# Performance work log

Measured on AMD Instinct MI355X. Metric: run time of the kernel, lower is better.

The kernel has to match this reference:

```python
import jax, jax.numpy as jnp
import numpy as np

# ActivationWithGain: activation scaled so a standard-normal input keeps unit variance.
_s = np.random.default_rng(0).standard_normal(1 << 20).astype(np.float32)
GAIN = float(1.0 / (_s / (1.0 + np.exp(-_s))).std())  # SiLU gain ~ 1.787
INV_SQRT2 = np.float32(1.0 / np.sqrt(2.0))


def _act(x):
    return jax.nn.silu(x) * jnp.float32(GAIN)


def setup_inputs() -> dict:
    key = jax.random.key(0)
    ks = jax.random.split(key, 9)
    n_up, n_dn, n_nuc, dim, edim = 512, 512, 256, 256, 32
    n_el = n_up + n_dn
    n_edges = n_el * n_nuc  # dense electron-nucleus bipartite graph
    return {
        "elec_emb": jax.random.normal(ks[0], (n_el, dim), jnp.float32),
        "up_inp": jax.random.normal(ks[1], (n_nuc, dim), jnp.float32),
        "down_inp": jax.random.normal(ks[2], (n_nuc, dim), jnp.float32),
        "edge_emb": jax.random.normal(ks[3], (n_edges, edim), jnp.float32),
        "contr": jax.random.uniform(ks[4], (n_edges,), jnp.float32),
        "norm": jax.random.uniform(ks[5], (n_el,), jnp.float32),
        "W_out": jax.random.normal(ks[6], (dim, dim), jnp.float32) / np.float32(np.sqrt(dim)),
        "b_out": jnp.zeros((dim,), jnp.float32),
        "W_edge": jax.random.normal(ks[7], (edim, dim), jnp.float32) / np.float32(np.sqrt(edim)),
        "W_out2": jax.random.normal(ks[8], (dim, dim), jnp.float32) / np.float32(np.sqrt(dim)),
        "b_out2": jnp.zeros((dim,), jnp.float32),
        "scale1": jnp.ones((), jnp.float32),  # FixedScalingFactor (frozen after init)
        "scale2": jnp.ones((), jnp.float32),
        "n_up": n_up,
        "n_down": n_dn,
        "n_nuclei": n_nuc,
    }


def reference(elec_emb, up_inp, down_inp, edge_emb, contr, norm,
              W_out, b_out, W_edge, W_out2, b_out2, scale1, scale2,
              n_up, n_down, n_nuclei):
    n_el = n_up + n_down
    # adj_idx for a single graph: dense bipartite edges, sorted by electron index
    e_n_i = jnp.repeat(jnp.arange(n_el), n_nuclei)   # [E] electron index per edge
    e_n_k = jnp.tile(jnp.arange(n_nuclei), n_el)     # [E] nucleus index per edge

    out_emb = elec_emb @ W_out + b_out               # Dense(out_dim)

    mask = jnp.arange(n_el) < n_up                   # spin_mask: True for spin-up electrons
    e_n_mask = mask[e_n_i]
    # gather nuclear embeddings per edge, selecting up/down table by electron spin
    inp = jnp.where(e_n_mask[:, None], up_inp[e_n_k], down_inp[e_n_k])  # [E, D]

    weights = edge_emb @ W_edge                      # Dense_no_bias(out_dim), [E, D]
    # FixedScalingFactor: contr only weights the init-time variance estimate;
    # at runtime the op is x * scale1.
    to_elec = inp * weights * scale1                 # [E, D]

    agg = jax.ops.segment_sum(to_elec, e_n_i, num_segments=n_el,
                              indices_are_sorted=True)  # [n_el, D]
    out_emb = (out_emb + agg * norm[:, None]) * scale2
    out_emb = _act(out_emb)
    out_emb = _act(out_emb @ W_out2 + b_out2)
    # residual: shapes match, so rescaled sum
    return (elec_emb + out_emb) * INV_SQRT2
```

## Files before the change

### kernel.cpp

```cpp
#include <hip/hip_runtime.h>
#include <hip/hip_bf16.h>

#define N_EL   1024
#define N_UP   512
#define NNUC   256
#define DIM    256
#define EDIM   32
#define KTOT   8192
#define NKP    8

#define GAIN_F      1.7872135f
#define INV_SQRT2_F 0.7071067811865476f

typedef __attribute__((ext_vector_type(8))) short bf16x8;
typedef __attribute__((ext_vector_type(4))) short bf16x4;
typedef __attribute__((ext_vector_type(4))) float f32x4;

__device__ __forceinline__ short f2bf(float x) {
    union { __hip_bfloat16 h; short s; } u;
    u.h = __float2bfloat16(x);
    return u.s;
}

__global__ __launch_bounds__(256) void prep_kernel(
    const float* __restrict__ up, const float* __restrict__ dn,
    const float* __restrict__ wedge,
    const float* __restrict__ w1, const float* __restrict__ w2,
    const float* __restrict__ elec,
    short* __restrict__ w1f, short* __restrict__ w2f,
    short* __restrict__ elecb, short* __restrict__ Tf)
{
    const int idx = (blockIdx.x << 8) + threadIdx.x;

    if (idx < 65536) {
        {
            const int b  = idx & 7;
            const int l  = (idx >> 3) & 63;
            const int q  = (idx >> 9) & 7;
            const int nt = idx >> 12;
            const int j  = (q << 5) + ((l >> 4) << 3) + b;
            const int d  = (nt << 4) + (l & 15);
            w1f[idx] = f2bf(w1[j * DIM + d]);
            w2f[idx] = f2bf(w2[j * DIM + d]);
        }
        {
            const f32x4 v = *(const f32x4*)(elec + (idx << 2));
            bf16x4 o;
            o[0] = f2bf(v[0]); o[1] = f2bf(v[1]);
            o[2] = f2bf(v[2]); o[3] = f2bf(v[3]);
            *(bf16x4*)(elecb + (idx << 2)) = o;
        }
    }

    {
        const int s   = idx >> 18;
        const int rem = idx & 262143;
        const int kt  = rem >> 10;
        const int dt  = (rem >> 6) & 15;
        const int l   = rem & 63;
        const int d   = (dt << 4) + (l & 15);
        const int jb  = (l >> 4) << 3;
        const float* __restrict__ inp = s ? dn : up;
        const float iv = inp[kt * DIM + d];
        const float* __restrict__ wcol = wedge + d;
        bf16x8 o;
        #pragma unroll
        for (int b = 0; b < 8; ++b)
            o[b] = f2bf(iv * wcol[(jb + b) * DIM]);
        *(bf16x8*)(Tf + ((size_t)s << 21) + ((size_t)rem << 3)) = o;
    }
}

__global__ __launch_bounds__(512) void edge_gemm(
    const float* __restrict__ eemb,
    const short* __restrict__ Tf,
    float* __restrict__ P)
{
    __shared__ short A_lds[2][4096];

    const int tid  = threadIdx.x;
    const int w    = tid >> 6;
    const int lane = tid & 63;
    const int g    = lane >> 4;
    const int c    = lane & 15;
    const int kp   = blockIdx.x & 7;
    const int rt   = blockIdx.x >> 3;
    const int rb   = rt << 5;
    const int kb   = kp << 10;

    const short* __restrict__ Tb = Tf + ((rb < N_UP) ? 0 : (1 << 21));

    const int f  = w;
    const int r_ = f >> 2;
    const int q_ = f & 3;
    const float* __restrict__ Asrc = eemb
        + (size_t)(rb + (r_ << 4) + c) * KTOT
        + kb + (q_ << 5) + (g << 3);

    f32x4 s_lo, s_hi;
    bf16x8 bA[8], bB[8];

    auto STAGE_LOAD = [&](int sub) {
        const float* p = Asrc + (sub << 7);
        s_lo = *(const f32x4*)p;
        s_hi = *(const f32x4*)(p + 4);
    };
    auto STAGE_WRITE = [&](int buf) {
        union { bf16x8 v; short s[8]; } o;
        o.s[0] = f2bf(s_lo[0]); o.s[1] = f2bf(s_lo[1]);
        o.s[2] = f2bf(s_lo[2]); o.s[3] = f2bf(s_lo[3]);
        o.s[4] = f2bf(s_hi[0]); o.s[5] = f2bf(s_hi[1]);
        o.s[6] = f2bf(s_hi[2]); o.s[7] = f2bf(s_hi[3]);
        *(bf16x8*)(&A_lds[buf][(f << 9) + (lane << 3)]) = o.v;
    };
    auto LOADB = [&](int sub, bf16x8 (&bd)[8]) {
        #pragma unroll
        for (int t = 0; t < 2; ++t) {
            const int ct = (w << 1) + t;
            #pragma unroll
            for (int q = 0; q < 4; ++q) {
                const int ktg = (kp << 5) + (sub << 2) + q;
                bd[(t << 2) + q] = *(const bf16x8*)(
                    Tb + (((((ktg << 4) + ct) << 6) + lane) << 3));
            }
        }
    };

    f32x4 acc[2][2] = {{{0.f,0.f,0.f,0.f},{0.f,0.f,0.f,0.f}},
                       {{0.f,0.f,0.f,0.f},{0.f,0.f,0.f,0.f}}};

    auto COMPUTE = [&](int buf, bf16x8 (&bc)[8]) {
        bf16x8 a[2][4];
        #pragma unroll
        for (int rr = 0; rr < 2; ++rr)
            #pragma unroll
            for (int q = 0; q < 4; ++q)
                a[rr][q] = *(const bf16x8*)(
                    &A_lds[buf][((((rr << 2) + q)) << 9) + (lane << 3)]);
        #pragma unroll
        for (int q = 0; q < 4; ++q) {
            acc[0][0] = __builtin_amdgcn_mfma_f32_16x16x32_bf16(a[0][q], bc[q],     acc[0][0], 0, 0, 0);
            acc[0][1] = __builtin_amdgcn_mfma_f32_16x16x32_bf16(a[0][q], bc[4 + q], acc[0][1], 0, 0, 0);
            acc[1][0] = __builtin_amdgcn_mfma_f32_16x16x32_bf16(a[1][q], bc[q],     acc[1][0], 0, 0, 0);
            acc[1][1] = __builtin_amdgcn_mfma_f32_16x16x32_bf16(a[1][q], bc[4 + q], acc[1][1], 0, 0, 0);
        }
    };

    STAGE_LOAD(0);
    LOADB(0, bA);
    STAGE_WRITE(0);
    __syncthreads();

    #pragma unroll
    for (int sub = 0; sub < 8; ++sub) {
        if ((sub & 1) == 0) {
            if (sub < 7) { STAGE_LOAD(sub + 1); LOADB(sub + 1, bB); }
            COMPUTE(0, bA);
        } else {
            if (sub < 7) { STAGE_LOAD(sub + 1); LOADB(sub + 1, bA); }
            COMPUTE(1, bB);
        }
        if (sub < 7) STAGE_WRITE((sub & 1) ^ 1);
        __syncthreads();
    }

    float* __restrict__ Pp = P + ((size_t)kp << 18);
    #pragma unroll
    for (int rr = 0; rr < 2; ++rr)
        #pragma unroll
        for (int t = 0; t < 2; ++t) {
            const int ct = (w << 1) + t;
            #pragma unroll
            for (int j = 0; j < 4; ++j) {
                const int row = rb + (rr << 4) + (g << 2) + j;
                Pp[(row << 8) + (ct << 4) + c] = acc[rr][t][j];
            }
        }
}

__global__ __launch_bounds__(256) void reduce_kernel(
    const float* __restrict__ P,
    const float* __restrict__ s1p,
    float* __restrict__ agg)
{
    const int idx = (blockIdx.x << 8) + threadIdx.x;
    const float s1 = *s1p;
    f32x4 s = {0.f, 0.f, 0.f, 0.f};
    #pragma unroll
    for (int kp = 0; kp < NKP; ++kp) {
        const f32x4 v = *(const f32x4*)(P + ((size_t)kp << 18) + (idx << 2));
        s[0] += v[0]; s[1] += v[1]; s[2] += v[2]; s[3] += v[3];
    }
    s[0] *= s1; s[1] *= s1; s[2] *= s1; s[3] *= s1;
    *(f32x4*)(agg + (idx << 2)) = s;
}

__global__ __launch_bounds__(512) void out_kernel(
    const short* __restrict__ elecb,
    const short* __restrict__ w1f, const short* __restrict__ w2f,
    const float* __restrict__ elec, const float* __restrict__ agg,
    const float* __restrict__ norm,
    const float* __restrict__ b1, const float* __restrict__ b2,
    const float* __restrict__ s2p,
    float* __restrict__ outp)
{
    __shared__ short h_s[16][264];

    const int tid  = threadIdx.x;
    const int w    = tid >> 6;
    const int lane = tid & 63;
    const int g    = lane >> 4;
    const int c    = lane & 15;
    const int mt   = blockIdx.x >> 2;
    const int qd   = blockIdx.x & 3;
    const int mb   = mt << 4;

    const short* abase = elecb + ((mb + c) << 8) + (g << 3);
    bf16x8 a[8];
    #pragma unroll
    for (int q = 0; q < 8; ++q) a[q] = *(const bf16x8*)(abase + (q << 5));

    const float s2 = *s2p;

    #pragma unroll
    for (int t = 0; t < 2; ++t) {
        const int ct = (w << 1) + t;
        const short* bb = w1f + (ct << 12) + (lane << 3);
        bf16x8 b[8];
        #pragma unroll
        for (int q = 0; q < 8; ++q) b[q] = *(const bf16x8*)(bb + (q << 9));
        f32x4 acc = {0.f, 0.f, 0.f, 0.f};
        #pragma unroll
        for (int q = 0; q < 8; ++q)
            acc = __builtin_amdgcn_mfma_f32_16x16x32_bf16(a[q], b[q], acc, 0, 0, 0);

        const int n  = (ct << 4) + c;
        const float bv = b1[n];
        #pragma unroll
        for (int r = 0; r < 4; ++r) {
            const int mr = (g << 2) + r;
            const int m  = mb + mr;
            const float y = (acc[r] + bv + agg[(m << 8) + n] * norm[m]) * s2;
            const float sig = 1.f / (1.f + __expf(-y));
            h_s[mr][n] = f2bf(GAIN_F * y * sig);
        }
    }
    __syncthreads();

    if (w < 4) {
        bf16x8 a2[8];
        #pragma unroll
        for (int q = 0; q < 8; ++q)
            a2[q] = *(const bf16x8*)(&h_s[c][(q << 5) + (g << 3)]);

        const int ct = (qd << 2) + w;
        const short* bb = w2f + (ct << 12) + (lane << 3);
        bf16x8 b[8];
        #pragma unroll
        for (int q = 0; q < 8; ++q) b[q] = *(const bf16x8*)(bb + (q << 9));
        f32x4 acc = {0.f, 0.f, 0.f, 0.f};
        #pragma unroll
        for (int q = 0; q < 8; ++q)
            acc = __builtin_amdgcn_mfma_f32_16x16x32_bf16(a2[q], b[q], acc, 0, 0, 0);

        const int n  = (ct << 4) + c;
        const float bv = b2[n];
        #pragma unroll
        for (int r = 0; r < 4; ++r) {
            const int m = mb + (g << 2) + r;
            const float z = acc[r] + bv;
            const float sig = 1.f / (1.f + __expf(-z));
            const float o = GAIN_F * z * sig;
            outp[(m << 8) + n] = (elec[(m << 8) + n] + o) * INV_SQRT2_F;
        }
    }
}

extern "C" void kernel_launch(void* const* d_in, const int* in_sizes, int n_in,
                              void* d_out, int out_size, void* d_ws, size_t ws_size,
                              hipStream_t stream)
{
    const float* elec  = (const float*)d_in[0];
    const float* up    = (const float*)d_in[1];
    const float* dn    = (const float*)d_in[2];
    const float* eemb  = (const float*)d_in[3];
    const float* norm  = (const float*)d_in[5];
    const float* W1    = (const float*)d_in[6];
    const float* b1    = (const float*)d_in[7];
    const float* Wedge = (const float*)d_in[8];
    const float* W2    = (const float*)d_in[9];
    const float* b2    = (const float*)d_in[10];
    const float* s1    = (const float*)d_in[11];
    const float* s2    = (const float*)d_in[12];

    short* sbase = (short*)d_ws;
    short* w1f   = sbase;
    short* w2f   = sbase + 65536;
    short* elecb = sbase + 131072;
    short* Tf    = sbase + 393216;
    float* P     = (float*)(sbase + 393216 + 4194304);
    float* agg   = P + (size_t)NKP * 262144;

    prep_kernel  <<<2048, 256, 0, stream>>>(up, dn, Wedge, W1, W2, elec,
                                            w1f, w2f, elecb, Tf);
    edge_gemm    <<<256, 512, 0, stream>>>(eemb, Tf, P);
    reduce_kernel<<<256, 256, 0, stream>>>(P, s1, agg);
    out_kernel   <<<256, 512, 0, stream>>>(elecb, w1f, w2f, elec, agg, norm,
                                           b1, b2, s2, (float*)d_out);
}
```

Before: 30.99 us.

## Pre-convert edge embeddings to MFMA-tiled bf16 in prep, drop LDS staging

The fp32 edge_emb matrix is now converted once in the prep kernel into a bf16 layout already tiled for MFMA fragments. The edge GEMM then loads A fragments straight from global memory into registers with double buffering, which removes the LDS staging buffer and the per-step __syncthreads. The cost is an extra full pass over the 32 MB fp32 input to write a 16 MB bf16 copy, plus twice as many prep blocks. Since the GEMM reads A only once per block anyway, the extra traffic may outweigh the sync savings.

```diff
diff --git a/kernel.cpp b/kernel.cpp
--- a/kernel.cpp
+++ b/kernel.cpp
@@ -26,9 +26,10 @@
     const float* __restrict__ up, const float* __restrict__ dn,
     const float* __restrict__ wedge,
     const float* __restrict__ w1, const float* __restrict__ w2,
-    const float* __restrict__ elec,
+    const float* __restrict__ elec, const float* __restrict__ eemb,
     short* __restrict__ w1f, short* __restrict__ w2f,
-    short* __restrict__ elecb, short* __restrict__ Tf)
+    short* __restrict__ elecb, short* __restrict__ Tf,
+    short* __restrict__ eembb)
 {
     const int idx = (blockIdx.x << 8) + threadIdx.x;
 
@@ -52,7 +53,7 @@
         }
     }
 
-    {
+    if (idx < 524288) {
         const int s   = idx >> 18;
         const int rem = idx & 262143;
         const int kt  = rem >> 10;
@@ -69,15 +70,30 @@
             o[b] = f2bf(iv * wcol[(jb + b) * DIM]);
         *(bf16x8*)(Tf + ((size_t)s << 21) + ((size_t)rem << 3)) = o;
     }
+
+    {
+        const int mt16 = idx >> 14;
+        const int kt   = (idx >> 6) & 255;
+        const int l    = idx & 63;
+        const int row  = (mt16 << 4) + (l & 15);
+        const int kk   = (kt << 5) + ((l >> 4) << 3);
+        const float* src = eemb + (size_t)row * KTOT + kk;
+        const f32x4 lo = *(const f32x4*)src;
+        const f32x4 hi = *(const f32x4*)(src + 4);
+        bf16x8 o;
+        o[0] = f2bf(lo[0]); o[1] = f2bf(lo[1]);
+        o[2] = f2bf(lo[2]); o[3] = f2bf(lo[3]);
+        o[4] = f2bf(hi[0]); o[5] = f2bf(hi[1]);
+        o[6] = f2bf(hi[2]); o[7] = f2bf(hi[3]);
+        *(bf16x8*)(eembb + ((size_t)idx << 3)) = o;
+    }
 }
 
 __global__ __launch_bounds__(512) void edge_gemm(
-    const float* __restrict__ eemb,
+    const short* __restrict__ eembb,
     const short* __restrict__ Tf,
     float* __restrict__ P)
 {
-    __shared__ short A_lds[2][4096];
-
     const int tid  = threadIdx.x;
     const int w    = tid >> 6;
     const int lane = tid & 63;
@@ -86,32 +102,20 @@
     const int kp   = blockIdx.x & 7;
     const int rt   = blockIdx.x >> 3;
     const int rb   = rt << 5;
-    const int kb   = kp << 10;
 
     const short* __restrict__ Tb = Tf + ((rb < N_UP) ? 0 : (1 << 21));
 
-    const int f  = w;
-    const int r_ = f >> 2;
-    const int q_ = f & 3;
-    const float* __restrict__ Asrc = eemb
-        + (size_t)(rb + (r_ << 4) + c) * KTOT
-        + kb + (q_ << 5) + (g << 3);
-
-    f32x4 s_lo, s_hi;
-    bf16x8 bA[8], bB[8];
-
-    auto STAGE_LOAD = [&](int sub) {
-        const float* p = Asrc + (sub << 7);
-        s_lo = *(const f32x4*)p;
-        s_hi = *(const f32x4*)(p + 4);
-    };
-    auto STAGE_WRITE = [&](int buf) {
-        union { bf16x8 v; short s[8]; } o;
-        o.s[0] = f2bf(s_lo[0]); o.s[1] = f2bf(s_lo[1]);
-        o.s[2] = f2bf(s_lo[2]); o.s[3] = f2bf(s_lo[3]);
-        o.s[4] = f2bf(s_hi[0]); o.s[5] = f2bf(s_hi[1]);
-        o.s[6] = f2bf(s_hi[2]); o.s[7] = f2bf(s_hi[3]);
-        *(bf16x8*)(&A_lds[buf][(f << 9) + (lane << 3)]) = o.v;
+    auto LOADA = [&](int sub, bf16x8 (&ad)[2][4]) {
+        #pragma unroll
+        for (int rr = 0; rr < 2; ++rr) {
+            const int mt16 = (rt << 1) + rr;
+            #pragma unroll
+            for (int q = 0; q < 4; ++q) {
+                const int kt = (kp << 5) + (sub << 2) + q;
+                ad[rr][q] = *(const bf16x8*)(
+                    eembb + ((size_t)(((mt16 << 8) + kt) << 6) + lane) * 8);
+            }
+        }
     };
     auto LOADB = [&](int sub, bf16x8 (&bd)[8]) {
         #pragma unroll
@@ -129,14 +133,7 @@
     f32x4 acc[2][2] = {{{0.f,0.f,0.f,0.f},{0.f,0.f,0.f,0.f}},
                        {{0.f,0.f,0.f,0.f},{0.f,0.f,0.f,0.f}}};
 
-    auto COMPUTE = [&](int buf, bf16x8 (&bc)[8]) {
-        bf16x8 a[2][4];
-        #pragma unroll
-        for (int rr = 0; rr < 2; ++rr)
-            #pragma unroll
-            for (int q = 0; q < 4; ++q)
-                a[rr][q] = *(const bf16x8*)(
-                    &A_lds[buf][((((rr << 2) + q)) << 9) + (lane << 3)]);
+    auto COMPUTE = [&](bf16x8 (&a)[2][4], bf16x8 (&bc)[8]) {
         #pragma unroll
         for (int q = 0; q < 4; ++q) {
             acc[0][0] = __builtin_amdgcn_mfma_f32_16x16x32_bf16(a[0][q], bc[q],     acc[0][0], 0, 0, 0);
@@ -146,22 +143,20 @@
         }
     };
 
-    STAGE_LOAD(0);
+    bf16x8 aA[2][4], aB[2][4], bA[8], bB[8];
+
+    LOADA(0, aA);
     LOADB(0, bA);
-    STAGE_WRITE(0);
-    __syncthreads();
 
     #pragma unroll
     for (int sub = 0; sub < 8; ++sub) {
         if ((sub & 1) == 0) {
-            if (sub < 7) { STAGE_LOAD(sub + 1); LOADB(sub + 1, bB); }
-            COMPUTE(0, bA);
+            if (sub < 7) { LOADA(sub + 1, aB); LOADB(sub + 1, bB); }
+            COMPUTE(aA, bA);
         } else {
-            if (sub < 7) { STAGE_LOAD(sub + 1); LOADB(sub + 1, bA); }
-            COMPUTE(1, bB);
-        }
-        if (sub < 7) STAGE_WRITE((sub & 1) ^ 1);
-        __syncthreads();
+            if (sub < 7) { LOADA(sub + 1, aA); LOADB(sub + 1, bA); }
+            COMPUTE(aB, bB);
+        }
     }
 
     float* __restrict__ Pp = P + ((size_t)kp << 18);
@@ -298,12 +293,13 @@
     short* w2f   = sbase + 65536;
     short* elecb = sbase + 131072;
     short* Tf    = sbase + 393216;
-    float* P     = (float*)(sbase + 393216 + 4194304);
+    short* eembb = sbase + 393216 + 4194304;
+    float* P     = (float*)(sbase + 393216 + 4194304 + 8388608);
     float* agg   = P + (size_t)NKP * 262144;
 
-    prep_kernel  <<<2048, 256, 0, stream>>>(up, dn, Wedge, W1, W2, elec,
-                                            w1f, w2f, elecb, Tf);
-    edge_gemm    <<<256, 512, 0, stream>>>(eemb, Tf, P);
+    prep_kernel  <<<4096, 256, 0, stream>>>(up, dn, Wedge, W1, W2, elec, eemb,
+                                            w1f, w2f, elecb, Tf, eembb);
+    edge_gemm    <<<256, 512, 0, stream>>>(eembb, Tf, P);
     reduce_kernel<<<256, 256, 0, stream>>>(P, s1, agg);
     out_kernel   <<<256, 512, 0, stream>>>(elecb, w1f, w2f, elec, agg, norm,
                                            b1, b2, s2, (float*)d_out);
```

After: 35.37 us. 14.1% more time.
